# Kernel optimization log

Measured on AMD Instinct MI355X. Metric: run time of the kernel, lower is better.

The kernel has to match this reference:

```python
import jax, jax.numpy as jnp
import numpy as np

N = 100000   # nodes
E = 1600000  # edges
D = 128      # input feature dim
H = 128      # hidden dim
C = 40       # output classes


def _gcn_conv(x, W, b, src, dst, norm):
    # PyG GCNConv: h = x @ W; out_i = sum_j (d_i^-1/2 d_j^-1/2) h_j over in-edges,
    # including self-loops, then + bias. norm = deg^-1/2 with self-loop-augmented degree.
    h = x @ W                                    # [N, H]
    coef = norm[src] * norm[dst]                 # [E]
    agg = jax.ops.segment_sum(h[src] * coef[:, None], dst, num_segments=N)
    agg = agg + h * (norm * norm)[:, None]       # self-loop term
    return agg + b


def setup_inputs() -> dict:
    key = jax.random.key(0)
    ks = jax.random.split(key, 12)
    x = jax.random.normal(ks[0], (N, D), dtype=jnp.float32)
    edge_index = jax.random.randint(ks[1], (2, E), 0, N, dtype=jnp.int64)

    def lin(k, fan_in, fan_out):
        s = 1.0 / np.sqrt(fan_in)
        return jax.random.uniform(k, (fan_in, fan_out), jnp.float32, -s, s)

    return {
        "x": x,
        "edge_index": edge_index,
        "W1": lin(ks[2], D, H), "b1": jnp.zeros((H,), jnp.float32),
        "W2": lin(ks[3], H, H), "b2": jnp.zeros((H,), jnp.float32),
        "W3": lin(ks[4], H, H), "b3": jnp.zeros((H,), jnp.float32),
        "Wp1": lin(ks[5], H, H), "bp1": jnp.zeros((H,), jnp.float32),
        "Wp2": lin(ks[6], H, C), "bp2": jnp.zeros((C,), jnp.float32),
    }


def reference(x, edge_index, W1, b1, W2, b2, W3, b3, Wp1, bp1, Wp2, bp2):
    src, dst = edge_index[0], edge_index[1]
    # degree with self-loops (GCNConv adds self-loops by default)
    deg = jax.ops.segment_sum(jnp.ones((E,), jnp.float32), dst, num_segments=N) + 1.0
    norm = jax.lax.rsqrt(deg)                    # deg^-1/2

    h = x
    for W, b in ((W1, b1), (W2, b2), (W3, b3)):
        h = _gcn_conv(h, W, b, src, dst, norm)
        h = jax.nn.relu(h)
        # dropout is a no-op at inference / rate 0

    h = h @ Wp1 + bp1
    h = h @ Wp2 + bp2
    return jax.nn.log_softmax(h, axis=1)
```

## Files before the change

kernel.cpp:

```cpp
#include <hip/hip_runtime.h>
#include <hip/hip_bf16.h>
#include <math.h>


#define DH 128
#define NC 40
#define BN 256
#define MAXNB 512
#define CH 8192
#define ECAP 6144
#define SP 136

typedef __attribute__((ext_vector_type(8))) short bf16x8;
typedef __attribute__((ext_vector_type(4))) float f32x4;

__device__ __forceinline__ unsigned short f2bf(float f) {
    unsigned u = __float_as_uint(f);
    unsigned r = (u + 0x7fffu + ((u >> 16) & 1u)) >> 16;
    return (unsigned short)r;
}
__device__ __forceinline__ unsigned pack2(float lo, float hi) {
    return (unsigned)f2bf(lo) | ((unsigned)f2bf(hi) << 16);
}


__global__ __launch_bounds__(256) void bucket_hist(const int* __restrict__ dst, int E,
                                                   unsigned* __restrict__ bcnt) {
    __shared__ unsigned h[MAXNB];
    int tid = threadIdx.x;
    for (int i = tid; i < MAXNB; i += 256) h[i] = 0;
    __syncthreads();
    int e0 = blockIdx.x * CH;
    int e1 = min(e0 + CH, E);
    for (int i = e0 + tid; i < e1; i += 256)
        atomicAdd(&h[dst[i] >> 8], 1u);
    __syncthreads();
    for (int i = tid; i < MAXNB; i += 256)
        if (h[i]) atomicAdd(&bcnt[i], h[i]);
}

__global__ __launch_bounds__(256) void bucket_alloc(const unsigned* __restrict__ bcnt,
                                                    unsigned* __restrict__ bbase,
                                                    unsigned* __restrict__ bpos,
                                                    unsigned* __restrict__ cursor, int NB) {
    int i = blockIdx.x * 256 + threadIdx.x;
    if (i < NB) {
        unsigned c = bcnt[i];
        unsigned o = atomicAdd(cursor, c);
        bbase[i] = o;
        bpos[i] = o;
    }
}

__global__ __launch_bounds__(256) void bucket_scatter(const int* __restrict__ src,
                                                      const int* __restrict__ dst, int E,
                                                      unsigned* __restrict__ bpos,
                                                      unsigned* __restrict__ ebuf) {
    __shared__ unsigned hist[MAXNB];
    __shared__ unsigned lbase[MAXNB];
    __shared__ unsigned gbase[MAXNB];
    __shared__ unsigned cur[MAXNB];
    __shared__ unsigned sorted[CH];
    __shared__ unsigned short sbkt[CH];
    __shared__ unsigned total;

    int tid = threadIdx.x;
    int e0 = blockIdx.x * CH;
    int nE = min(CH, E - e0);

    for (int i = tid; i < MAXNB; i += 256) { hist[i] = 0; cur[i] = 0; }
    if (tid == 0) total = 0;
    __syncthreads();

    for (int i = tid; i < nE; i += 256)
        atomicAdd(&hist[dst[e0 + i] >> 8], 1u);
    __syncthreads();

    for (int i = tid; i < MAXNB; i += 256) {
        unsigned h = hist[i];
        lbase[i] = h ? atomicAdd(&total, h) : 0u;
        gbase[i] = h ? atomicAdd(&bpos[i], h) : 0u;
    }
    __syncthreads();

    for (int i = tid; i < nE; i += 256) {
        int s = src[e0 + i];
        int d = dst[e0 + i];
        unsigned b = (unsigned)d >> 8;
        unsigned r = atomicAdd(&cur[b], 1u);
        unsigned p = lbase[b] + r;
        sorted[p] = ((unsigned)s << 8) | ((unsigned)d & 255u);
        sbkt[p] = (unsigned short)b;
    }
    __syncthreads();

    for (int p = tid; p < nE; p += 256) {
        unsigned b = sbkt[p];
        ebuf[gbase[b] + (p - lbase[b])] = sorted[p];
    }
}


__global__ __launch_bounds__(256) void bucket_deg(const unsigned* __restrict__ ebuf,
                                                  const unsigned* __restrict__ bbase,
                                                  const unsigned* __restrict__ bcnt,
                                                  unsigned* __restrict__ cnt,
                                                  float* __restrict__ nrm,
                                                  unsigned* __restrict__ dh, int N) {
    __shared__ unsigned h[BN];
    __shared__ unsigned dhh[256];
    int b = blockIdx.x, tid = threadIdx.x;
    unsigned ebase = bbase[b], ecnt = bcnt[b];
    h[tid] = 0; dhh[tid] = 0;
    __syncthreads();
    for (unsigned i = tid; i < ecnt; i += 256)
        atomicAdd(&h[ebuf[ebase + i] & 255u], 1u);
    __syncthreads();
    int node = b * BN + tid;
    unsigned myh = h[tid];
    if (node < N) {
        cnt[node] = myh;
        nrm[node] = rsqrtf((float)myh + 1.0f);
        atomicAdd(&dhh[min(myh, 255u)], 1u);
    }
    __syncthreads();
    if (dhh[tid]) atomicAdd(&dh[tid], dhh[tid]);
}

__global__ __launch_bounds__(256) void deg_scan(const unsigned* __restrict__ dh,
                                                unsigned* __restrict__ binpos,
                                                unsigned* __restrict__ nstart0,
                                                unsigned* __restrict__ estart) {
    __shared__ unsigned s[256];
    int t = threadIdx.x;
    s[t] = dh[t];
    __syncthreads();
    unsigned ns = 0, es = 0;
    for (int d = t + 1; d < 256; ++d) { ns += s[d]; es += s[d] * (unsigned)d; }
    binpos[t] = ns;
    nstart0[t] = ns;
    estart[t] = es;
}

__global__ __launch_bounds__(256) void deg_scatter(const unsigned* __restrict__ cnt, int N,
                                                   unsigned* __restrict__ binpos,
                                                   const unsigned* __restrict__ nstart0,
                                                   const unsigned* __restrict__ estart,
                                                   int* __restrict__ perm,
                                                   unsigned* __restrict__ pd2,
                                                   unsigned* __restrict__ offN) {
    __shared__ unsigned h[256], base[256], cur[256], sns[256], ses[256];
    int t = threadIdx.x;
    h[t] = 0; cur[t] = 0; sns[t] = nstart0[t]; ses[t] = estart[t];
    __syncthreads();
    int i = blockIdx.x * 256 + t;
    unsigned d = 0;
    if (i < N) { d = min(cnt[i], 255u); atomicAdd(&h[d], 1u); }
    __syncthreads();
    if (h[t]) base[t] = atomicAdd(&binpos[t], h[t]);
    __syncthreads();
    if (i < N) {
        unsigned r = atomicAdd(&cur[d], 1u);
        unsigned idx = base[d] + r;
        unsigned off2 = ses[d] + (idx - sns[d]) * d;
        perm[idx] = i;
        pd2[idx] = (off2 << 9) | d;
        offN[i] = off2;
    }
}


__global__ __launch_bounds__(256) void bucket_fill(const unsigned* __restrict__ ebuf,
                                                   const unsigned* __restrict__ bbase,
                                                   const unsigned* __restrict__ bcnt,
                                                   const unsigned* __restrict__ offN,
                                                   int* __restrict__ csr, int N) {
    __shared__ unsigned h[BN], lb[BN], cur[BN], ofs[BN];
    __shared__ int lcsr[ECAP];
    __shared__ unsigned char snl[ECAP];
    __shared__ unsigned tot;

    int b = blockIdx.x, tid = threadIdx.x;
    unsigned ebase = bbase[b], ecnt = bcnt[b];
    int node = b * BN + tid;
    h[tid] = 0; cur[tid] = 0;
    ofs[tid] = (node < N) ? offN[node] : 0u;
    if (tid == 0) tot = 0;
    __syncthreads();

    for (unsigned i = tid; i < ecnt; i += 256)
        atomicAdd(&h[ebuf[ebase + i] & 255u], 1u);
    __syncthreads();

    unsigned myh = h[tid];
    lb[tid] = myh ? atomicAdd(&tot, myh) : 0u;
    __syncthreads();

    if (ecnt <= ECAP) {
        for (unsigned i = tid; i < ecnt; i += 256) {
            unsigned v = ebuf[ebase + i];
            unsigned nl = v & 255u;
            unsigned r = atomicAdd(&cur[nl], 1u);
            unsigned p = lb[nl] + r;
            lcsr[p] = (int)(v >> 8);
            snl[p] = (unsigned char)nl;
        }
        __syncthreads();
        for (unsigned i = tid; i < ecnt; i += 256) {
            unsigned nl = snl[i];
            csr[ofs[nl] + (i - lb[nl])] = lcsr[i];
        }
    } else {
        for (unsigned i = tid; i < ecnt; i += 256) {
            unsigned v = ebuf[ebase + i];
            unsigned nl = v & 255u;
            unsigned r = atomicAdd(&cur[nl], 1u);
            csr[ofs[nl] + r] = (int)(v >> 8);
        }
    }
}


__global__ __launch_bounds__(256) void prep_w(const float* __restrict__ W1,
                                              const float* __restrict__ W2,
                                              const float* __restrict__ W3,
                                              const float* __restrict__ Wp1,
                                              const float* __restrict__ bp1,
                                              const float* __restrict__ Wp2,
                                              const float* __restrict__ bp2,
                                              unsigned short* __restrict__ Wt,
                                              unsigned short* __restrict__ Wft,
                                              float* __restrict__ bfh) {
    int id = blockIdx.x * 256 + threadIdx.x;
    if (id < 3 * DH * DH) {
        int l = id >> 14, r = id & (DH * DH - 1);
        int k = r >> 7, n = r & 127;
        const float* W = (l == 0) ? W1 : (l == 1) ? W2 : W3;
        Wt[l * DH * DH + n * DH + k] = f2bf(W[k * DH + n]);
    } else if (id < 3 * DH * DH + 48 * DH) {
        int o = id - 3 * DH * DH;
        int c = o >> 7, k = o & 127;
        float acc = 0.f;
        if (c < NC)
            for (int j = 0; j < DH; ++j) acc += Wp1[k * DH + j] * Wp2[j * NC + c];
        Wft[c * DH + k] = f2bf(acc);
    } else if (id < 3 * DH * DH + 48 * DH + 48) {
        int c = id - 3 * DH * DH - 48 * DH;
        float acc = 0.f;
        if (c < NC) {
            acc = bp2[c];
            for (int j = 0; j < DH; ++j) acc += bp1[j] * Wp2[j * NC + c];
        }
        bfh[c] = acc;
    }
}


__global__ __launch_bounds__(256) void gemm_mfma_f32(const float* __restrict__ X,
                                                     const unsigned short* __restrict__ Wt,
                                                     const float* __restrict__ nrm,
                                                     unsigned short* __restrict__ outb,
                                                     int nrows) {
    const int tid = threadIdx.x;
    const int wave = tid >> 6;
    const int lane = tid & 63;
    const int m = lane & 15;
    const int quad = lane >> 4;
    const int rbase = blockIdx.x * 128 + wave * 32;

    union U8 { bf16x8 v; unsigned u[4]; };

    f32x4 acc[2][8];
#pragma unroll
    for (int rt = 0; rt < 2; ++rt)
#pragma unroll
        for (int ct = 0; ct < 8; ++ct) acc[rt][ct] = (f32x4){0.f, 0.f, 0.f, 0.f};

#pragma unroll
    for (int kt = 0; kt < 4; ++kt) {
        const int kof = kt * 32 + quad * 8;
        bf16x8 a[2], b[8];
#pragma unroll
        for (int rt = 0; rt < 2; ++rt) {
            int r = rbase + rt * 16 + m;
            r = (r < nrows) ? r : (nrows - 1);
            const float* p = X + (size_t)r * DH + kof;
            float4 u0 = *(const float4*)p;
            float4 u1 = *(const float4*)(p + 4);
            U8 t;
            t.u[0] = pack2(u0.x, u0.y);
            t.u[1] = pack2(u0.z, u0.w);
            t.u[2] = pack2(u1.x, u1.y);
            t.u[3] = pack2(u1.z, u1.w);
            a[rt] = t.v;
        }
#pragma unroll
        for (int ct = 0; ct < 8; ++ct)
            b[ct] = *(const bf16x8*)(Wt + (ct * 16 + m) * DH + kof);
#pragma unroll
        for (int rt = 0; rt < 2; ++rt)
#pragma unroll
            for (int ct = 0; ct < 8; ++ct)
                acc[rt][ct] = __builtin_amdgcn_mfma_f32_16x16x32_bf16(a[rt], b[ct], acc[rt][ct], 0, 0, 0);
    }

#pragma unroll
    for (int rt = 0; rt < 2; ++rt)
#pragma unroll
        for (int reg = 0; reg < 4; ++reg) {
            int r = rbase + rt * 16 + quad * 4 + reg;
            if (r < nrows) {
                float s = nrm[r];
#pragma unroll
                for (int ct = 0; ct < 8; ++ct)
                    outb[(size_t)r * DH + ct * 16 + m] = f2bf(acc[rt][ct][reg] * s);
            }
        }
}


__device__ __forceinline__ void bf8_add(float* acc, uint4 v) {
    acc[0] += __uint_as_float(v.x << 16);
    acc[1] += __uint_as_float(v.x & 0xffff0000u);
    acc[2] += __uint_as_float(v.y << 16);
    acc[3] += __uint_as_float(v.y & 0xffff0000u);
    acc[4] += __uint_as_float(v.z << 16);
    acc[5] += __uint_as_float(v.z & 0xffff0000u);
    acc[6] += __uint_as_float(v.w << 16);
    acc[7] += __uint_as_float(v.w & 0xffff0000u);
}

__device__ __forceinline__ void gather_phase(const uint4* __restrict__ Abf,
                                             const int* __restrict__ csr,
                                             const unsigned* __restrict__ pd2,
                                             const int* __restrict__ perm,
                                             const float* __restrict__ bias,
                                             unsigned short (*sA)[SP],
                                             int* snode, float* snrm, int N) {
    const int tid = threadIdx.x;
    const int g = tid >> 4;
    const int lane = tid & 15;
    const int idx = blockIdx.x * 16 + g;
    if (idx < N) {
        const unsigned pd = pd2[idx];
        const unsigned o = pd >> 9;
        const unsigned d = pd & 511u;
        const int node = perm[idx];

        float acc[8];
        {
            uint4 v = Abf[(size_t)node * 16 + lane];
            acc[0] = __uint_as_float(v.x << 16);
            acc[1] = __uint_as_float(v.x & 0xffff0000u);
            acc[2] = __uint_as_float(v.y << 16);
            acc[3] = __uint_as_float(v.y & 0xffff0000u);
            acc[4] = __uint_as_float(v.z << 16);
            acc[5] = __uint_as_float(v.z & 0xffff0000u);
            acc[6] = __uint_as_float(v.w << 16);
            acc[7] = __uint_as_float(v.w & 0xffff0000u);
        }

        unsigned e = 0;
        for (; e + 4 <= d; e += 4) {
            int s0 = csr[o + e + 0];
            int s1 = csr[o + e + 1];
            int s2 = csr[o + e + 2];
            int s3 = csr[o + e + 3];
            uint4 v0 = Abf[(size_t)s0 * 16 + lane];
            uint4 v1 = Abf[(size_t)s1 * 16 + lane];
            uint4 v2 = Abf[(size_t)s2 * 16 + lane];
            uint4 v3 = Abf[(size_t)s3 * 16 + lane];
            bf8_add(acc, v0);
            bf8_add(acc, v1);
            bf8_add(acc, v2);
            bf8_add(acc, v3);
        }
        for (; e < d; ++e) {
            int s = csr[o + e];
            uint4 v = Abf[(size_t)s * 16 + lane];
            bf8_add(acc, v);
        }

        float nm = rsqrtf((float)d + 1.0f);
        if (lane == 0) { snode[g] = node; snrm[g] = nm; }
        float4 b0 = *(const float4*)(bias + lane * 8);
        float4 b1 = *(const float4*)(bias + lane * 8 + 4);
        uint4 ov;
        ov.x = pack2(fmaxf(acc[0] * nm + b0.x, 0.f), fmaxf(acc[1] * nm + b0.y, 0.f));
        ov.y = pack2(fmaxf(acc[2] * nm + b0.z, 0.f), fmaxf(acc[3] * nm + b0.w, 0.f));
        ov.z = pack2(fmaxf(acc[4] * nm + b1.x, 0.f), fmaxf(acc[5] * nm + b1.y, 0.f));
        ov.w = pack2(fmaxf(acc[6] * nm + b1.z, 0.f), fmaxf(acc[7] * nm + b1.w, 0.f));
        *(uint4*)&sA[g][lane * 8] = ov;
    }
    __syncthreads();
}


__global__ __launch_bounds__(256) void agg_gemm(const uint4* __restrict__ Abf,
                                                const int* __restrict__ csr,
                                                const unsigned* __restrict__ pd2,
                                                const int* __restrict__ perm,
                                                const float* __restrict__ bias,
                                                const unsigned short* __restrict__ Wt,
                                                unsigned short* __restrict__ outb, int N) {
    __shared__ unsigned short sA[16][SP];
    __shared__ int snode[16];
    __shared__ float snrm[16];
    gather_phase(Abf, csr, pd2, perm, bias, sA, snode, snrm, N);

    const int tid = threadIdx.x;
    const int wave = tid >> 6;
    const int l64 = tid & 63;
    const int m = l64 & 15;
    const int quad = l64 >> 4;

    f32x4 acc[2];
    acc[0] = (f32x4){0.f, 0.f, 0.f, 0.f};
    acc[1] = (f32x4){0.f, 0.f, 0.f, 0.f};

#pragma unroll
    for (int kt = 0; kt < 4; ++kt) {
        const int kof = kt * 32 + quad * 8;
        bf16x8 a = *(const bf16x8*)&sA[m][kof];
#pragma unroll
        for (int c2 = 0; c2 < 2; ++c2) {
            const int ct = wave * 2 + c2;
            bf16x8 b = *(const bf16x8*)(Wt + (ct * 16 + m) * DH + kof);
            acc[c2] = __builtin_amdgcn_mfma_f32_16x16x32_bf16(a, b, acc[c2], 0, 0, 0);
        }
    }

#pragma unroll
    for (int reg = 0; reg < 4; ++reg) {
        int idx = blockIdx.x * 16 + quad * 4 + reg;
        if (idx < N) {
            int r = snode[quad * 4 + reg];
            float s = snrm[quad * 4 + reg];
#pragma unroll
            for (int c2 = 0; c2 < 2; ++c2)
                outb[(size_t)r * DH + (wave * 2 + c2) * 16 + m] = f2bf(acc[c2][reg] * s);
        }
    }
}


__global__ __launch_bounds__(256) void agg_head(const uint4* __restrict__ Abf,
                                                const int* __restrict__ csr,
                                                const unsigned* __restrict__ pd2,
                                                const int* __restrict__ perm,
                                                const float* __restrict__ bias,
                                                const unsigned short* __restrict__ Wft,
                                                const float* __restrict__ bfh,
                                                float* __restrict__ out, int N) {
    __shared__ unsigned short sA[16][SP];
    __shared__ int snode[16];
    __shared__ float snrm[16];
    gather_phase(Abf, csr, pd2, perm, bias, sA, snode, snrm, N);

    const int tid = threadIdx.x;
    if (tid >= 64) return;
    const int m = tid & 15;
    const int quad = tid >> 4;

    f32x4 acc[3];
#pragma unroll
    for (int ct = 0; ct < 3; ++ct) acc[ct] = (f32x4){0.f, 0.f, 0.f, 0.f};

#pragma unroll
    for (int kt = 0; kt < 4; ++kt) {
        const int kof = kt * 32 + quad * 8;
        bf16x8 a = *(const bf16x8*)&sA[m][kof];
#pragma unroll
        for (int ct = 0; ct < 3; ++ct) {
            bf16x8 b = *(const bf16x8*)(Wft + (ct * 16 + m) * DH + kof);
            acc[ct] = __builtin_amdgcn_mfma_f32_16x16x32_bf16(a, b, acc[ct], 0, 0, 0);
        }
    }

    float bias0 = bfh[m];
    float bias1 = bfh[16 + m];
    float bias2 = bfh[32 + m];

#pragma unroll
    for (int reg = 0; reg < 4; ++reg) {
        float v0 = acc[0][reg] + bias0;
        float v1 = acc[1][reg] + bias1;
        float v2 = (m < 8) ? (acc[2][reg] + bias2) : -1e30f;
        float mx = fmaxf(fmaxf(v0, v1), v2);
#pragma unroll
        for (int dlt = 1; dlt < 16; dlt <<= 1) mx = fmaxf(mx, __shfl_xor(mx, dlt));
        float s = __expf(v0 - mx) + __expf(v1 - mx) + ((m < 8) ? __expf(v2 - mx) : 0.f);
#pragma unroll
        for (int dlt = 1; dlt < 16; dlt <<= 1) s += __shfl_xor(s, dlt);
        float ls = mx + __logf(s);
        int idx = blockIdx.x * 16 + quad * 4 + reg;
        if (idx < N) {
            int r = snode[quad * 4 + reg];
            out[(size_t)r * NC + m] = v0 - ls;
            out[(size_t)r * NC + 16 + m] = v1 - ls;
            if (m < 8) out[(size_t)r * NC + 32 + m] = v2 - ls;
        }
    }
}


extern "C" void kernel_launch(void* const* d_in, const int* in_sizes, int n_in,
                              void* d_out, int out_size, void* d_ws, size_t ws_size,
                              hipStream_t stream) {
    const float* x   = (const float*)d_in[0];
    const int*   ei  = (const int*)d_in[1];
    const float* W1  = (const float*)d_in[2];
    const float* b1  = (const float*)d_in[3];
    const float* W2  = (const float*)d_in[4];
    const float* b2  = (const float*)d_in[5];
    const float* W3  = (const float*)d_in[6];
    const float* b3  = (const float*)d_in[7];
    const float* Wp1 = (const float*)d_in[8];
    const float* bp1 = (const float*)d_in[9];
    const float* Wp2 = (const float*)d_in[10];
    const float* bp2 = (const float*)d_in[11];
    float* out = (float*)d_out;

    const int N = in_sizes[0] / DH;
    const int E = in_sizes[1] / 2;
    const int* src = ei;
    const int* dst = ei + E;
    const int NB = (N + BN - 1) / BN;

    char* w = (char*)d_ws;
    unsigned short* Ab  = (unsigned short*)w; w += (size_t)N * DH * 2;
    unsigned short* Bb  = (unsigned short*)w; w += (size_t)N * DH * 2;
    int*      csr    = (int*)w;      w += (size_t)E * 4;
    unsigned* ebuf   = (unsigned*)w; w += (size_t)E * 4;
    unsigned* bcnt   = (unsigned*)w; w += MAXNB * 4;
    unsigned* cursor = (unsigned*)w; w += 16;
    unsigned* dh     = (unsigned*)w; w += 256 * 4;
    unsigned* bbase  = (unsigned*)w; w += MAXNB * 4;
    unsigned* bpos   = (unsigned*)w; w += MAXNB * 4;
    unsigned* binpos = (unsigned*)w; w += 256 * 4;
    unsigned* nstart0= (unsigned*)w; w += 256 * 4;
    unsigned* estart = (unsigned*)w; w += 256 * 4;
    unsigned* cnt    = (unsigned*)w; w += (size_t)N * 4;
    float*    nrm    = (float*)w;    w += (size_t)N * 4;
    unsigned* offN   = (unsigned*)w; w += (size_t)N * 4;
    unsigned* pd2    = (unsigned*)w; w += (size_t)((N + 31) & ~31) * 4;
    int*      perm   = (int*)w;      w += (size_t)((N + 31) & ~31) * 4;
    unsigned short* Wt  = (unsigned short*)w; w += 3 * DH * DH * 2;
    unsigned short* Wft = (unsigned short*)w; w += 48 * DH * 2;
    float*    bfh    = (float*)w;    w += 64 * 4;

    const int gC = (E + CH - 1) / CH;
    const int gN = (N + 255) / 256;

    hipMemsetAsync(bcnt, 0, MAXNB * 4 + 16 + 256 * 4, stream);
    bucket_hist   <<<gC, 256, 0, stream>>>(dst, E, bcnt);
    bucket_alloc  <<<(NB + 255) / 256, 256, 0, stream>>>(bcnt, bbase, bpos, cursor, NB);
    bucket_scatter<<<gC, 256, 0, stream>>>(src, dst, E, bpos, ebuf);
    bucket_deg    <<<NB, 256, 0, stream>>>(ebuf, bbase, bcnt, cnt, nrm, dh, N);
    deg_scan      <<<1, 256, 0, stream>>>(dh, binpos, nstart0, estart);
    deg_scatter   <<<gN, 256, 0, stream>>>(cnt, N, binpos, nstart0, estart, perm, pd2, offN);
    bucket_fill   <<<NB, 256, 0, stream>>>(ebuf, bbase, bcnt, offN, csr, N);
    prep_w<<<(3 * DH * DH + 48 * DH + 48 + 255) / 256, 256, 0, stream>>>(
        W1, W2, W3, Wp1, bp1, Wp2, bp2, Wt, Wft, bfh);

    const int gG = (N + 127) / 128;
    const int gF = (N + 15) / 16;

    gemm_mfma_f32<<<gG, 256, 0, stream>>>(x, Wt, nrm, Ab, N);
    agg_gemm<<<gF, 256, 0, stream>>>((const uint4*)Ab, csr, pd2, perm, b1,
                                     Wt + DH * DH, Bb, N);
    agg_gemm<<<gF, 256, 0, stream>>>((const uint4*)Bb, csr, pd2, perm, b2,
                                     Wt + 2 * DH * DH, Ab, N);
    agg_head<<<gF, 256, 0, stream>>>((const uint4*)Ab, csr, pd2, perm, b3,
                                     Wft, bfh, out, N);
}
```

Measured before the change: 418.0 us.

## Shrink node buckets, drop LDS staging in scatter, fold degree scan, prefetch CSR indices

Halves the bucket width to 128 nodes, so there are twice as many buckets with smaller per-block edge chunks and LDS buffers. The bucket scatter now writes edges straight to global memory instead of staging and sorting them in shared memory first. The single-block degree-scan kernel is removed and its prefix sums are recomputed redundantly in every deg_scatter block. The aggregation loop gains an 8-wide software-pipelined gather that prefetches the next CSR indices while the current feature rows load. This trades fewer launches and more memory-level parallelism for less coalesced ebuf writes and half-idle threads in the per-bucket kernels.

```diff
diff --git a/kernel.cpp b/kernel.cpp
--- a/kernel.cpp
+++ b/kernel.cpp
@@ -5,10 +5,10 @@
 
 #define DH 128
 #define NC 40
-#define BN 256
-#define MAXNB 512
-#define CH 8192
-#define ECAP 6144
+#define BN 128
+#define MAXNB 1024
+#define CH 4096
+#define ECAP 3072
 #define SP 136
 
 typedef __attribute__((ext_vector_type(8))) short bf16x8;
@@ -33,7 +33,7 @@
     int e0 = blockIdx.x * CH;
     int e1 = min(e0 + CH, E);
     for (int i = e0 + tid; i < e1; i += 256)
-        atomicAdd(&h[dst[i] >> 8], 1u);
+        atomicAdd(&h[(unsigned)dst[i] >> 7], 1u);
     __syncthreads();
     for (int i = tid; i < MAXNB; i += 256)
         if (h[i]) atomicAdd(&bcnt[i], h[i]);
@@ -57,46 +57,28 @@
                                                       unsigned* __restrict__ bpos,
                                                       unsigned* __restrict__ ebuf) {
     __shared__ unsigned hist[MAXNB];
-    __shared__ unsigned lbase[MAXNB];
     __shared__ unsigned gbase[MAXNB];
     __shared__ unsigned cur[MAXNB];
-    __shared__ unsigned sorted[CH];
-    __shared__ unsigned short sbkt[CH];
-    __shared__ unsigned total;
-
     int tid = threadIdx.x;
     int e0 = blockIdx.x * CH;
     int nE = min(CH, E - e0);
 
     for (int i = tid; i < MAXNB; i += 256) { hist[i] = 0; cur[i] = 0; }
-    if (tid == 0) total = 0;
-    __syncthreads();
-
+    __syncthreads();
     for (int i = tid; i < nE; i += 256)
-        atomicAdd(&hist[dst[e0 + i] >> 8], 1u);
-    __syncthreads();
-
+        atomicAdd(&hist[(unsigned)dst[e0 + i] >> 7], 1u);
+    __syncthreads();
     for (int i = tid; i < MAXNB; i += 256) {
         unsigned h = hist[i];
-        lbase[i] = h ? atomicAdd(&total, h) : 0u;
         gbase[i] = h ? atomicAdd(&bpos[i], h) : 0u;
     }
     __syncthreads();
-
     for (int i = tid; i < nE; i += 256) {
         int s = src[e0 + i];
         int d = dst[e0 + i];
-        unsigned b = (unsigned)d >> 8;
+        unsigned b = (unsigned)d >> 7;
         unsigned r = atomicAdd(&cur[b], 1u);
-        unsigned p = lbase[b] + r;
-        sorted[p] = ((unsigned)s << 8) | ((unsigned)d & 255u);
-        sbkt[p] = (unsigned short)b;
-    }
-    __syncthreads();
-
-    for (int p = tid; p < nE; p += 256) {
-        unsigned b = sbkt[p];
-        ebuf[gbase[b] + (p - lbase[b])] = sorted[p];
+        ebuf[gbase[b] + r] = ((unsigned)s << 7) | ((unsigned)d & 127u);
     }
 }
 
@@ -111,53 +93,43 @@
     __shared__ unsigned dhh[256];
     int b = blockIdx.x, tid = threadIdx.x;
     unsigned ebase = bbase[b], ecnt = bcnt[b];
-    h[tid] = 0; dhh[tid] = 0;
+    if (tid < BN) h[tid] = 0;
+    dhh[tid] = 0;
     __syncthreads();
     for (unsigned i = tid; i < ecnt; i += 256)
-        atomicAdd(&h[ebuf[ebase + i] & 255u], 1u);
-    __syncthreads();
-    int node = b * BN + tid;
-    unsigned myh = h[tid];
-    if (node < N) {
-        cnt[node] = myh;
-        nrm[node] = rsqrtf((float)myh + 1.0f);
-        atomicAdd(&dhh[min(myh, 255u)], 1u);
+        atomicAdd(&h[ebuf[ebase + i] & 127u], 1u);
+    __syncthreads();
+    if (tid < BN) {
+        int node = b * BN + tid;
+        if (node < N) {
+            unsigned myh = h[tid];
+            cnt[node] = myh;
+            nrm[node] = rsqrtf((float)myh + 1.0f);
+            atomicAdd(&dhh[min(myh, 255u)], 1u);
+        }
     }
     __syncthreads();
     if (dhh[tid]) atomicAdd(&dh[tid], dhh[tid]);
 }
 
-__global__ __launch_bounds__(256) void deg_scan(const unsigned* __restrict__ dh,
-                                                unsigned* __restrict__ binpos,
-                                                unsigned* __restrict__ nstart0,
-                                                unsigned* __restrict__ estart) {
-    __shared__ unsigned s[256];
-    int t = threadIdx.x;
-    s[t] = dh[t];
-    __syncthreads();
-    unsigned ns = 0, es = 0;
-    for (int d = t + 1; d < 256; ++d) { ns += s[d]; es += s[d] * (unsigned)d; }
-    binpos[t] = ns;
-    nstart0[t] = ns;
-    estart[t] = es;
-}
-
 __global__ __launch_bounds__(256) void deg_scatter(const unsigned* __restrict__ cnt, int N,
+                                                   const unsigned* __restrict__ dh,
                                                    unsigned* __restrict__ binpos,
-                                                   const unsigned* __restrict__ nstart0,
-                                                   const unsigned* __restrict__ estart,
                                                    int* __restrict__ perm,
                                                    unsigned* __restrict__ pd2,
                                                    unsigned* __restrict__ offN) {
-    __shared__ unsigned h[256], base[256], cur[256], sns[256], ses[256];
+    __shared__ unsigned h[256], base[256], cur[256], sdh[256], sns[256], ses[256];
     int t = threadIdx.x;
-    h[t] = 0; cur[t] = 0; sns[t] = nstart0[t]; ses[t] = estart[t];
-    __syncthreads();
+    h[t] = 0; cur[t] = 0; sdh[t] = dh[t];
+    __syncthreads();
+    unsigned ns = 0, es = 0;
+    for (int d = t + 1; d < 256; ++d) { ns += sdh[d]; es += sdh[d] * (unsigned)d; }
+    sns[t] = ns; ses[t] = es;
     int i = blockIdx.x * 256 + t;
     unsigned d = 0;
     if (i < N) { d = min(cnt[i], 255u); atomicAdd(&h[d], 1u); }
     __syncthreads();
-    if (h[t]) base[t] = atomicAdd(&binpos[t], h[t]);
+    if (h[t]) base[t] = sns[t] + atomicAdd(&binpos[t], h[t]);
     __syncthreads();
     if (i < N) {
         unsigned r = atomicAdd(&cur[d], 1u);
@@ -182,27 +154,31 @@
 
     int b = blockIdx.x, tid = threadIdx.x;
     unsigned ebase = bbase[b], ecnt = bcnt[b];
-    int node = b * BN + tid;
-    h[tid] = 0; cur[tid] = 0;
-    ofs[tid] = (node < N) ? offN[node] : 0u;
+    if (tid < BN) {
+        int node = b * BN + tid;
+        h[tid] = 0; cur[tid] = 0;
+        ofs[tid] = (node < N) ? offN[node] : 0u;
+    }
     if (tid == 0) tot = 0;
     __syncthreads();
 
     for (unsigned i = tid; i < ecnt; i += 256)
-        atomicAdd(&h[ebuf[ebase + i] & 255u], 1u);
-    __syncthreads();
-
-    unsigned myh = h[tid];
-    lb[tid] = myh ? atomicAdd(&tot, myh) : 0u;
+        atomicAdd(&h[ebuf[ebase + i] & 127u], 1u);
+    __syncthreads();
+
+    if (tid < BN) {
+        unsigned myh = h[tid];
+        lb[tid] = myh ? atomicAdd(&tot, myh) : 0u;
+    }
     __syncthreads();
 
     if (ecnt <= ECAP) {
         for (unsigned i = tid; i < ecnt; i += 256) {
             unsigned v = ebuf[ebase + i];
-            unsigned nl = v & 255u;
+            unsigned nl = v & 127u;
             unsigned r = atomicAdd(&cur[nl], 1u);
             unsigned p = lb[nl] + r;
-            lcsr[p] = (int)(v >> 8);
+            lcsr[p] = (int)(v >> 7);
             snl[p] = (unsigned char)nl;
         }
         __syncthreads();
@@ -213,9 +189,9 @@
     } else {
         for (unsigned i = tid; i < ecnt; i += 256) {
             unsigned v = ebuf[ebase + i];
-            unsigned nl = v & 255u;
+            unsigned nl = v & 127u;
             unsigned r = atomicAdd(&cur[nl], 1u);
-            csr[ofs[nl] + r] = (int)(v >> 8);
+            csr[ofs[nl] + r] = (int)(v >> 7);
         }
     }
 }
@@ -361,6 +337,43 @@
         }
 
         unsigned e = 0;
+        if (d >= 8) {
+            int c0 = csr[o + 0], c1 = csr[o + 1], c2 = csr[o + 2], c3 = csr[o + 3];
+            int c4 = csr[o + 4], c5 = csr[o + 5], c6 = csr[o + 6], c7 = csr[o + 7];
+            for (; e + 16 <= d; e += 8) {
+                uint4 v0 = Abf[(size_t)c0 * 16 + lane];
+                uint4 v1 = Abf[(size_t)c1 * 16 + lane];
+                uint4 v2 = Abf[(size_t)c2 * 16 + lane];
+                uint4 v3 = Abf[(size_t)c3 * 16 + lane];
+                uint4 v4 = Abf[(size_t)c4 * 16 + lane];
+                uint4 v5 = Abf[(size_t)c5 * 16 + lane];
+                uint4 v6 = Abf[(size_t)c6 * 16 + lane];
+                uint4 v7 = Abf[(size_t)c7 * 16 + lane];
+                c0 = csr[o + e + 8];  c1 = csr[o + e + 9];
+                c2 = csr[o + e + 10]; c3 = csr[o + e + 11];
+                c4 = csr[o + e + 12]; c5 = csr[o + e + 13];
+                c6 = csr[o + e + 14]; c7 = csr[o + e + 15];
+                bf8_add(acc, v0); bf8_add(acc, v1);
+                bf8_add(acc, v2); bf8_add(acc, v3);
+                bf8_add(acc, v4); bf8_add(acc, v5);
+                bf8_add(acc, v6); bf8_add(acc, v7);
+            }
+            {
+                uint4 v0 = Abf[(size_t)c0 * 16 + lane];
+                uint4 v1 = Abf[(size_t)c1 * 16 + lane];
+                uint4 v2 = Abf[(size_t)c2 * 16 + lane];
+                uint4 v3 = Abf[(size_t)c3 * 16 + lane];
+                uint4 v4 = Abf[(size_t)c4 * 16 + lane];
+                uint4 v5 = Abf[(size_t)c5 * 16 + lane];
+                uint4 v6 = Abf[(size_t)c6 * 16 + lane];
+                uint4 v7 = Abf[(size_t)c7 * 16 + lane];
+                bf8_add(acc, v0); bf8_add(acc, v1);
+                bf8_add(acc, v2); bf8_add(acc, v3);
+                bf8_add(acc, v4); bf8_add(acc, v5);
+                bf8_add(acc, v6); bf8_add(acc, v7);
+                e += 8;
+            }
+        }
         for (; e + 4 <= d; e += 4) {
             int s0 = csr[o + e + 0];
             int s1 = csr[o + e + 1];
@@ -535,11 +548,9 @@
     unsigned* bcnt   = (unsigned*)w; w += MAXNB * 4;
     unsigned* cursor = (unsigned*)w; w += 16;
     unsigned* dh     = (unsigned*)w; w += 256 * 4;
+    unsigned* binpos = (unsigned*)w; w += 256 * 4;
     unsigned* bbase  = (unsigned*)w; w += MAXNB * 4;
     unsigned* bpos   = (unsigned*)w; w += MAXNB * 4;
-    unsigned* binpos = (unsigned*)w; w += 256 * 4;
-    unsigned* nstart0= (unsigned*)w; w += 256 * 4;
-    unsigned* estart = (unsigned*)w; w += 256 * 4;
     unsigned* cnt    = (unsigned*)w; w += (size_t)N * 4;
     float*    nrm    = (float*)w;    w += (size_t)N * 4;
     unsigned* offN   = (unsigned*)w; w += (size_t)N * 4;
@@ -552,13 +563,12 @@
     const int gC = (E + CH - 1) / CH;
     const int gN = (N + 255) / 256;
 
-    hipMemsetAsync(bcnt, 0, MAXNB * 4 + 16 + 256 * 4, stream);
+    hipMemsetAsync(bcnt, 0, MAXNB * 4 + 16 + 256 * 4 + 256 * 4, stream);
     bucket_hist   <<<gC, 256, 0, stream>>>(dst, E, bcnt);
     bucket_alloc  <<<(NB + 255) / 256, 256, 0, stream>>>(bcnt, bbase, bpos, cursor, NB);
     bucket_scatter<<<gC, 256, 0, stream>>>(src, dst, E, bpos, ebuf);
     bucket_deg    <<<NB, 256, 0, stream>>>(ebuf, bbase, bcnt, cnt, nrm, dh, N);
-    deg_scan      <<<1, 256, 0, stream>>>(dh, binpos, nstart0, estart);
-    deg_scatter   <<<gN, 256, 0, stream>>>(cnt, N, binpos, nstart0, estart, perm, pd2, offN);
+    deg_scatter   <<<gN, 256, 0, stream>>>(cnt, N, dh, binpos, perm, pd2, offN);
     bucket_fill   <<<NB, 256, 0, stream>>>(ebuf, bbase, bcnt, offN, csr, N);
     prep_w<<<(3 * DH * DH + 48 * DH + 48 + 255) / 256, 256, 0, stream>>>(
         W1, W2, W3, Wp1, bp1, Wp2, bp2, Wt, Wft, bfh);
```

Measured after the change: 434.2 us. 3.9% more time.
